# Kernel tuning notes

Measured on AMD Instinct MI355X. Metric: run time of the kernel, lower is better.

## Reference

```python
import jax, jax.numpy as jnp
import numpy as np

# Constants from module-level env defaults
CONST_VAL = 10.0                       # VLLM_SOFTMAX_CONST_VAL
EPS = 1.1754943508222875e-38           # torch.finfo(torch.bfloat16).tiny
SCALE = 0.08838834764831845            # 1/sqrt(head_size=128)

B, QH, KVH, D = 32, 32, 8, 128         # batch, q heads, kv heads, head dim
NUM_CACHE_BLOCKS, BLOCK_SIZE = 600, 128
BLOCKS_PER_SEQ = 16                    # context 2048 / block_size 128
NB = B * BLOCKS_PER_SEQ                # 512 active blocks


def setup_inputs() -> dict:
    key = jax.random.key(0)
    ks = jax.random.split(key, 6)
    query = jax.random.normal(ks[0], (B, QH, D), dtype=jnp.float32)
    key_cache = jax.random.normal(ks[1], (NUM_CACHE_BLOCKS, BLOCK_SIZE, KVH, D), dtype=jnp.float32)
    value_cache = jax.random.normal(ks[2], (NUM_CACHE_BLOCKS, BLOCK_SIZE, KVH, D), dtype=jnp.float32)
    # each active block points at a distinct physical cache block
    block_list = jax.random.permutation(ks[3], NUM_CACHE_BLOCKS)[:NB].astype(jnp.int32)
    # block i belongs to sequence i // BLOCKS_PER_SEQ -> one-hot [NB, B]
    block_to_batch = jnp.arange(NB) // BLOCKS_PER_SEQ
    block_mapping = jax.nn.one_hot(block_to_batch, B, dtype=jnp.float32)
    # ALiBi-like per-position bias within each block (non-positive)
    block_bias = -5.0 * jax.random.uniform(ks[4], (NB, BLOCK_SIZE), dtype=jnp.float32)
    return {
        'query': query,
        'key_cache': key_cache,
        'value_cache': value_cache,
        'block_mapping': block_mapping,
        'block_bias': block_bias,
        'block_list': block_list,
    }


def reference(query, key_cache, value_cache, block_mapping, block_bias, block_list):
    """flat_pa decode path with the pa() const-norm softmax normalization (GQA)."""
    b, qh, d = query.shape
    kvh = key_cache.shape[2]
    g = qh // kvh                                   # queries per kv head
    nb, bs = block_bias.shape
    # batch2block(scale * query): [NB,B] @ [B, QH, D] -> [NB, QH, D]
    q = jnp.einsum('nb,bhd->nhd', block_mapping, SCALE * query)
    q = q.reshape(nb, kvh, g, 1, d)                 # [NB, KVH, G, 1, D]
    k = key_cache[block_list]                       # [NB, BS, KVH, D]
    v = value_cache[block_list]                     # [NB, BS, KVH, D]
    # attn = q @ k^T + block_bias : [NB, KVH, G, 1, BS]
    attn = jnp.einsum('nkgqd,nskd->nkgqs', q, k)
    attn = attn + block_bias[:, None, None, None, :]
    # const-norm exp (no running max; subtract fixed const)
    attn = jnp.exp(attn - CONST_VAL)
    block_sum = attn.sum(axis=-1, keepdims=True)    # [NB, KVH, G, 1, 1]
    # block2batch then batch2block: per-sequence sum broadcast back to blocks
    group_sums = jnp.einsum('nb,nkgqo->bkgqo', block_mapping, block_sum)
    group_sums = jnp.einsum('nb,bkgqo->nkgqo', block_mapping, group_sums) + EPS
    group_sums = jnp.maximum(block_sum, group_sums)
    attn = attn / group_sums
    out = jnp.einsum('nkgqs,nskd->nkgqd', attn, v)  # [NB, KVH, G, 1, D]
    # block2batch: accumulate per-block partial outputs into per-sequence output
    out = jnp.einsum('nb,nkgqd->bkgqd', block_mapping, out)
    return out.reshape(b, qh, d)                    # squeeze q-dim, flatten heads
```

## Files before the change

### kernel.cpp

```cpp
#include <hip/hip_runtime.h>

#define NBATCH 32
#define QH 32
#define KVH 8
#define G 4
#define DH 128
#define BS 128
#define NB 512
#define CONST_VAL 10.0f
#define EPS_T 1.1754943508222875e-38f
#define SCALE_F 0.08838834764831845f


__global__ void pa_zero_S(float* S) {
    int i = blockIdx.x * 256 + threadIdx.x;
    if (i < NBATCH * KVH * G) S[i] = 0.f;
}

__global__ __launch_bounds__(256) void pa_pass1(
    const float* __restrict__ query,
    const float* __restrict__ key_cache,
    const float* __restrict__ value_cache,
    const float* __restrict__ mapping,
    const float* __restrict__ bias,
    const int*   __restrict__ block_list,
    float* __restrict__ partial,
    float* __restrict__ bsum,
    float* __restrict__ S)
{
    const int n  = blockIdx.x;
    const int kh = blockIdx.y;
    const int t  = threadIdx.x;

    __shared__ float sW[NBATCH];
    __shared__ float sQ[G][DH];
    __shared__ float sKV[64][129];
    __shared__ float sE[G][BS];
    __shared__ float sBs[G];

    if (t < NBATCH) sW[t] = mapping[n * NBATCH + t];
    __syncthreads();

    {
        int i0 = t, i1 = t + 256;
        int g0 = i0 >> 7, d0 = i0 & 127;
        int g1 = i1 >> 7, d1 = i1 & 127;
        float qa = 0.f, qb = 0.f;
        for (int b = 0; b < NBATCH; ++b) {
            float w = sW[b];
            if (w != 0.f) {
                const float* qrow = query + ((size_t)b * QH + (size_t)kh * G) * DH;
                qa += w * qrow[g0 * DH + d0];
                qb += w * qrow[g1 * DH + d1];
            }
        }
        sQ[g0][d0] = qa * SCALE_F;
        sQ[g1][d1] = qb * SCALE_F;
    }

    const int p = block_list[n];
    const float* kbase = key_cache   + (size_t)p * BS * KVH * DH + (size_t)kh * DH;
    const float* vbase = value_cache + (size_t)p * BS * KVH * DH + (size_t)kh * DH;
    const int row_stride = KVH * DH;

    const int s_l = t & 63;
    const int g_s = t >> 6;
    for (int ph = 0; ph < 2; ++ph) {
        __syncthreads();
        for (int i = 0; i < 8; ++i) {
            int j = i * 256 + t;
            int row = j >> 5;
            int c4  = j & 31;
            float4 kv = *(const float4*)(kbase + (size_t)(ph * 64 + row) * row_stride + c4 * 4);
            float* dst = &sKV[row][c4 * 4];
            dst[0] = kv.x; dst[1] = kv.y; dst[2] = kv.z; dst[3] = kv.w;
        }
        __syncthreads();
        float acc = 0.f;
        #pragma unroll 8
        for (int d = 0; d < DH; ++d) acc += sKV[s_l][d] * sQ[g_s][d];
        int s = ph * 64 + s_l;
        sE[g_s][s] = __expf(acc + bias[(size_t)n * BS + s] - CONST_VAL);
    }
    __syncthreads();

    {
        int wave = t >> 6, lane = t & 63;
        float v = sE[wave][lane] + sE[wave][lane + 64];
        for (int off = 32; off > 0; off >>= 1) v += __shfl_down(v, off);
        if (lane == 0) sBs[wave] = v;
    }
    __syncthreads();
    if (t < G) {
        float bsv = sBs[t];
        bsum[((size_t)n * KVH + kh) * G + t] = bsv;
        for (int b = 0; b < NBATCH; ++b) {
            float w = sW[b];
            if (w != 0.f) atomicAdd(&S[(b * KVH + kh) * G + t], w * bsv);
        }
    }

    const int d_v = t & 127;
    const int gg  = t >> 7;
    float o0 = 0.f, o1 = 0.f;
    for (int ph = 0; ph < 2; ++ph) {
        __syncthreads();
        for (int i = 0; i < 8; ++i) {
            int j = i * 256 + t;
            int row = j >> 5;
            int c4  = j & 31;
            float4 vv = *(const float4*)(vbase + (size_t)(ph * 64 + row) * row_stride + c4 * 4);
            float* dst = &sKV[row][c4 * 4];
            dst[0] = vv.x; dst[1] = vv.y; dst[2] = vv.z; dst[3] = vv.w;
        }
        __syncthreads();
        int g0 = gg * 2, g1 = gg * 2 + 1;
        #pragma unroll 8
        for (int sl = 0; sl < 64; ++sl) {
            float v = sKV[sl][d_v];
            int s = ph * 64 + sl;
            o0 += sE[g0][s] * v;
            o1 += sE[g1][s] * v;
        }
    }
    size_t pb = (((size_t)n * KVH + kh) * G) * DH;
    partial[pb + (size_t)(gg * 2)     * DH + d_v] = o0;
    partial[pb + (size_t)(gg * 2 + 1) * DH + d_v] = o1;
}

__global__ __launch_bounds__(256) void pa_den(
    const float* __restrict__ mapping,
    const float* __restrict__ bsum,
    const float* __restrict__ S,
    float* __restrict__ den)
{
    int i = blockIdx.x * 256 + threadIdx.x;
    if (i >= NB * KVH * G) return;
    int g  = i & (G - 1);
    int kh = (i / G) & (KVH - 1);
    int n  = i / (G * KVH);
    float gs = 0.f;
    for (int b = 0; b < NBATCH; ++b)
        gs += mapping[n * NBATCH + b] * S[(b * KVH + kh) * G + g];
    gs += EPS_T;
    den[i] = fmaxf(bsum[i], gs);
}

__global__ __launch_bounds__(256) void pa_pass2(
    const float* __restrict__ mapping,
    const float* __restrict__ partial,
    const float* __restrict__ den,
    float* __restrict__ out)
{
    int b  = blockIdx.x;
    int kh = blockIdx.y;
    int t  = threadIdx.x;
    int g  = t >> 7;
    int d  = t & 127;

    __shared__ float sWc[NB];
    for (int i = t; i < NB; i += 256) sWc[i] = mapping[i * NBATCH + b];
    __syncthreads();

    float a0 = 0.f, a1 = 0.f;
    for (int n = 0; n < NB; ++n) {
        float w = sWc[n];
        if (w == 0.f) continue;
        int di = (n * KVH + kh) * G;
        size_t pb = (size_t)di * DH;
        a0 += w * partial[pb + (size_t)g * DH + d] / den[di + g];
        a1 += w * partial[pb + (size_t)(g + 2) * DH + d] / den[di + g + 2];
    }
    size_t ob = ((size_t)b * QH + (size_t)kh * G) * DH;
    out[ob + (size_t)g * DH + d]       = a0;
    out[ob + (size_t)(g + 2) * DH + d] = a1;
}

extern "C" void kernel_launch(void* const* d_in, const int* in_sizes, int n_in,
                              void* d_out, int out_size, void* d_ws, size_t ws_size,
                              hipStream_t stream) {
    const float* query       = (const float*)d_in[0];
    const float* key_cache   = (const float*)d_in[1];
    const float* value_cache = (const float*)d_in[2];
    const float* mapping     = (const float*)d_in[3];
    const float* bias        = (const float*)d_in[4];
    const int*   block_list  = (const int*)d_in[5];
    float* out = (float*)d_out;

    float* partial = (float*)d_ws;
    float* bsum    = partial + (size_t)NB * KVH * G * DH;
    float* S       = bsum + (size_t)NB * KVH * G;
    float* den     = S + (size_t)NBATCH * KVH * G;

    pa_zero_S<<<4, 256, 0, stream>>>(S);
    pa_pass1<<<dim3(NB, KVH), 256, 0, stream>>>(
        query, key_cache, value_cache, mapping, bias, block_list, partial, bsum, S);
    pa_den<<<(NB * KVH * G + 255) / 256, 256, 0, stream>>>(mapping, bsum, S, den);
    pa_pass2<<<dim3(NBATCH, KVH), 256, 0, stream>>>(mapping, partial, den, out);
}
```

Baseline: 642.1 us.

## Stream K/V directly into registers with DPP quad reductions in pass1

The pass1 kernel no longer stages K and V tiles through shared memory. Each thread loads float4 K/V rows directly from global memory, computes partial dot products against register-held queries, and reduces them with DPP quad swizzles plus a small shared-memory reduction. The PV product accumulates 16 register outputs per thread, followed by a shared cross-group reduction. The aim is to cut LDS traffic and barriers and to allow higher occupancy (launch bounds 256,7), at the cost of higher register pressure and extra reduction steps.

```diff
diff --git a/kernel.cpp b/kernel.cpp
--- a/kernel.cpp
+++ b/kernel.cpp
@@ -17,7 +17,19 @@
     if (i < NBATCH * KVH * G) S[i] = 0.f;
 }
 
-__global__ __launch_bounds__(256) void pa_pass1(
+__device__ __forceinline__ float dpp_xor1_add(float v) {
+    int sw = __builtin_amdgcn_update_dpp(0, __builtin_bit_cast(int, v), 0xB1, 0xF, 0xF, true);
+    return v + __builtin_bit_cast(float, sw);
+}
+__device__ __forceinline__ float dpp_xor2_add(float v) {
+    int sw = __builtin_amdgcn_update_dpp(0, __builtin_bit_cast(int, v), 0x4E, 0xF, 0xF, true);
+    return v + __builtin_bit_cast(float, sw);
+}
+__device__ __forceinline__ float quad_sum(float v) {
+    return dpp_xor2_add(dpp_xor1_add(v));
+}
+
+__global__ __launch_bounds__(256, 7) void pa_pass1(
     const float* __restrict__ query,
     const float* __restrict__ key_cache,
     const float* __restrict__ value_cache,
@@ -32,11 +44,11 @@
     const int kh = blockIdx.y;
     const int t  = threadIdx.x;
 
-    __shared__ float sW[NBATCH];
-    __shared__ float sQ[G][DH];
-    __shared__ float sKV[64][129];
-    __shared__ float sE[G][BS];
-    __shared__ float sBs[G];
+    __shared__ __align__(16) float sW[NBATCH];
+    __shared__ __align__(16) float sQ[G * 132];
+    __shared__ __align__(16) float sE[G * 132];
+    __shared__ __align__(16) float sBs[G];
+    __shared__ __align__(16) float uS[128 * 36];
 
     if (t < NBATCH) sW[t] = mapping[n * NBATCH + t];
     __syncthreads();
@@ -54,39 +66,55 @@
                 qb += w * qrow[g1 * DH + d1];
             }
         }
-        sQ[g0][d0] = qa * SCALE_F;
-        sQ[g1][d1] = qb * SCALE_F;
-    }
+        sQ[g0 * 132 + d0] = qa * SCALE_F;
+        sQ[g1 * 132 + d1] = qb * SCALE_F;
+    }
+    __syncthreads();
+
+    const int q4 = t & 31;
+    const int sg = t >> 5;
+
+    float4 qf0 = *(const float4*)&sQ[0 * 132 + q4 * 4];
+    float4 qf1 = *(const float4*)&sQ[1 * 132 + q4 * 4];
+    float4 qf2 = *(const float4*)&sQ[2 * 132 + q4 * 4];
+    float4 qf3 = *(const float4*)&sQ[3 * 132 + q4 * 4];
 
     const int p = block_list[n];
     const float* kbase = key_cache   + (size_t)p * BS * KVH * DH + (size_t)kh * DH;
     const float* vbase = value_cache + (size_t)p * BS * KVH * DH + (size_t)kh * DH;
     const int row_stride = KVH * DH;
 
-    const int s_l = t & 63;
-    const int g_s = t >> 6;
-    for (int ph = 0; ph < 2; ++ph) {
-        __syncthreads();
-        for (int i = 0; i < 8; ++i) {
-            int j = i * 256 + t;
-            int row = j >> 5;
-            int c4  = j & 31;
-            float4 kv = *(const float4*)(kbase + (size_t)(ph * 64 + row) * row_stride + c4 * 4);
-            float* dst = &sKV[row][c4 * 4];
-            dst[0] = kv.x; dst[1] = kv.y; dst[2] = kv.z; dst[3] = kv.w;
-        }
-        __syncthreads();
-        float acc = 0.f;
-        #pragma unroll 8
-        for (int d = 0; d < DH; ++d) acc += sKV[s_l][d] * sQ[g_s][d];
-        int s = ph * 64 + s_l;
-        sE[g_s][s] = __expf(acc + bias[(size_t)n * BS + s] - CONST_VAL);
+    #pragma unroll 4
+    for (int i = 0; i < 16; ++i) {
+        int s = sg * 16 + i;
+        float4 k = *(const float4*)(kbase + (size_t)s * row_stride + q4 * 4);
+        float p0 = k.x * qf0.x + k.y * qf0.y + k.z * qf0.z + k.w * qf0.w;
+        float p1 = k.x * qf1.x + k.y * qf1.y + k.z * qf1.z + k.w * qf1.w;
+        float p2 = k.x * qf2.x + k.y * qf2.y + k.z * qf2.z + k.w * qf2.w;
+        float p3 = k.x * qf3.x + k.y * qf3.y + k.z * qf3.z + k.w * qf3.w;
+        p0 = quad_sum(p0); p1 = quad_sum(p1); p2 = quad_sum(p2); p3 = quad_sum(p3);
+        if ((t & 3) == 0) {
+            *(float4*)&uS[s * 36 + (q4 >> 2) * 4] = make_float4(p0, p1, p2, p3);
+        }
+    }
+    __syncthreads();
+
+    {
+        int g = t & 3, sb = t >> 2;
+        #pragma unroll
+        for (int rep = 0; rep < 2; ++rep) {
+            int s = sb + rep * 64;
+            float acc = 0.f;
+            #pragma unroll
+            for (int j = 0; j < 8; ++j) acc += uS[s * 36 + j * 4 + g];
+            sE[g * 132 + s] = __expf(acc + bias[(size_t)n * BS + s] - CONST_VAL);
+        }
     }
     __syncthreads();
 
     {
         int wave = t >> 6, lane = t & 63;
-        float v = sE[wave][lane] + sE[wave][lane + 64];
+        float v = sE[wave * 132 + lane] + sE[wave * 132 + lane + 64];
         for (int off = 32; off > 0; off >>= 1) v += __shfl_down(v, off);
         if (lane == 0) sBs[wave] = v;
     }
@@ -100,32 +128,36 @@
         }
     }
 
-    const int d_v = t & 127;
-    const int gg  = t >> 7;
-    float o0 = 0.f, o1 = 0.f;
-    for (int ph = 0; ph < 2; ++ph) {
-        __syncthreads();
-        for (int i = 0; i < 8; ++i) {
-            int j = i * 256 + t;
-            int row = j >> 5;
-            int c4  = j & 31;
-            float4 vv = *(const float4*)(vbase + (size_t)(ph * 64 + row) * row_stride + c4 * 4);
-            float* dst = &sKV[row][c4 * 4];
-            dst[0] = vv.x; dst[1] = vv.y; dst[2] = vv.z; dst[3] = vv.w;
-        }
-        __syncthreads();
-        int g0 = gg * 2, g1 = gg * 2 + 1;
-        #pragma unroll 8
-        for (int sl = 0; sl < 64; ++sl) {
-            float v = sKV[sl][d_v];
-            int s = ph * 64 + sl;
-            o0 += sE[g0][s] * v;
-            o1 += sE[g1][s] * v;
-        }
-    }
-    size_t pb = (((size_t)n * KVH + kh) * G) * DH;
-    partial[pb + (size_t)(gg * 2)     * DH + d_v] = o0;
-    partial[pb + (size_t)(gg * 2 + 1) * DH + d_v] = o1;
+    float o00=0.f,o01=0.f,o02=0.f,o03=0.f;
+    float o10=0.f,o11=0.f,o12=0.f,o13=0.f;
+    float o20=0.f,o21=0.f,o22=0.f,o23=0.f;
+    float o30=0.f,o31=0.f,o32=0.f,o33=0.f;
+    #pragma unroll 4
+    for (int i = 0; i < 16; ++i) {
+        int s = sg * 16 + i;
+        float4 v = *(const float4*)(vbase + (size_t)s * row_stride + q4 * 4);
+        float e0 = sE[0 * 132 + s], e1 = sE[1 * 132 + s];
+        float e2 = sE[2 * 132 + s], e3 = sE[3 * 132 + s];
+        o00 += e0 * v.x; o01 += e0 * v.y; o02 += e0 * v.z; o03 += e0 * v.w;
+        o10 += e1 * v.x; o11 += e1 * v.y; o12 += e1 * v.z; o13 += e1 * v.w;
+        o20 += e2 * v.x; o21 += e2 * v.y; o22 += e2 * v.z; o23 += e2 * v.w;
+        o30 += e3 * v.x; o31 += e3 * v.y; o32 += e3 * v.z; o33 += e3 * v.w;
+    }
+    *(float4*)&uS[(sg * 4 + 0) * 132 + q4 * 4] = make_float4(o00, o01, o02, o03);
+    *(float4*)&uS[(sg * 4 + 1) * 132 + q4 * 4] = make_float4(o10, o11, o12, o13);
+    *(float4*)&uS[(sg * 4 + 2) * 132 + q4 * 4] = make_float4(o20, o21, o22, o23);
+    *(float4*)&uS[(sg * 4 + 3) * 132 + q4 * 4] = make_float4(o30, o31, o32, o33);
+    __syncthreads();
+
+    #pragma unroll
+    for (int rep = 0; rep < 2; ++rep) {
+        int idx = t + rep * 256;
+        int g = idx >> 7, d = idx & 127;
+        float acc = 0.f;
+        #pragma unroll
+        for (int sg2 = 0; sg2 < 8; ++sg2) acc += uS[(sg2 * 4 + g) * 132 + d];
+        partial[(((size_t)n * KVH + kh) * G + g) * DH + d] = acc;
+    }
 }
 
 __global__ __launch_bounds__(256) void pa_den(
```

After: 649.2 us. Within noise of the previous version (+1.1%).
